# Performance work log

Measured on AMD Instinct MI355X. Metric: run time of the kernel, lower is better.

The kernel has to match this reference:

```python
import jax, jax.numpy as jnp
import numpy as np

N_NODES = 100000
N_EDGES = 1600000
IN_CH = 512
MID_CH = 64   # hard-coded mid_layer_channel in the module
OUT_CH = 40


def setup_inputs() -> dict:
    key = jax.random.key(0)
    k0, k1, k2, k3 = jax.random.split(key, 4)
    node_feature = jax.random.normal(k0, (N_NODES, IN_CH), dtype=jnp.float32)
    # edge index [2, E]: row 0 = src, row 1 = dst
    adj_list = jax.random.randint(k1, (2, N_EDGES), 0, N_NODES, dtype=jnp.int32)
    # GCNConv parameters (Glorot-ish scale)
    W1 = jax.random.normal(k2, (IN_CH, MID_CH), dtype=jnp.float32) * (1.0 / np.sqrt(IN_CH))
    b1 = jnp.zeros((MID_CH,), dtype=jnp.float32)
    W2 = jax.random.normal(k3, (MID_CH, OUT_CH), dtype=jnp.float32) * (1.0 / np.sqrt(MID_CH))
    b2 = jnp.zeros((OUT_CH,), dtype=jnp.float32)
    return {"node_feature": node_feature, "adj_list": adj_list,
            "W1": W1, "b1": b1, "W2": W2, "b2": b2}


def _gcn_conv(x, W, b, src, dst, deg_inv_sqrt, n_nodes):
    # Standard GCNConv: D^{-1/2} (A + I) D^{-1/2} (x W) + b
    h = x @ W                                             # [N, F_out]
    norm = deg_inv_sqrt[src] * deg_inv_sqrt[dst]          # [E]
    agg = jax.ops.segment_sum(h[src] * norm[:, None], dst, num_segments=n_nodes)
    agg = agg + h * (deg_inv_sqrt * deg_inv_sqrt)[:, None]  # self-loop term
    return agg + b


def reference(node_feature, adj_list, W1, b1, W2, b2):
    n = node_feature.shape[0]
    src, dst = adj_list[0], adj_list[1]
    # degree with self-loops (in-degree at dst + 1)
    deg = jax.ops.segment_sum(jnp.ones_like(dst, dtype=node_feature.dtype), dst,
                              num_segments=n) + 1.0
    deg_inv_sqrt = jax.lax.rsqrt(deg)
    h = jax.nn.elu(_gcn_conv(node_feature, W1, b1, src, dst, deg_inv_sqrt, n))
    out = _gcn_conv(h, W2, b2, src, dst, deg_inv_sqrt, n)
    return jax.nn.log_softmax(out, axis=1)
```

## Files before the change

### kernel.cpp

```cpp
#include <hip/hip_runtime.h>
#include <hip/hip_bf16.h>
#include <math.h>

#define IN_CH 512
#define MID_CH 64
#define OUT_CH 40

typedef __attribute__((ext_vector_type(8))) short short8;
typedef __attribute__((ext_vector_type(4))) float f32x4;
typedef __attribute__((ext_vector_type(2))) float f32x2;

static __device__ __forceinline__ unsigned short f2bf(float f) {
    unsigned int u = __float_as_uint(f);
    u += 0x7fffu + ((u >> 16) & 1u);
    return (unsigned short)(u >> 16);
}

__global__ void k_init(const float* __restrict__ W1, unsigned short* __restrict__ w1f,
                       int* __restrict__ cnt, int* __restrict__ esrc, int dummy_off,
                       int epad, unsigned char* __restrict__ h1q,
                       unsigned char* __restrict__ h2q, int N) {
    int i = blockIdx.x * 256 + threadIdx.x;
    if (i < epad) esrc[i] = dummy_off;
    if (i < N) cnt[i] = 0;
    if (i < IN_CH * MID_CH) {
        int k = i >> 6, c = i & 63;
        w1f[(((k >> 3) * 64) + c) * 8 + (k & 7)] = f2bf(W1[i]);
    }
    if (i < 64) {
        h1q[(size_t)N * 64 + i] = 0;
        h2q[(size_t)N * 64 + i] = 0;
    }
}

__global__ void k_countrank(const int* __restrict__ dst, int* __restrict__ cnt,
                            int* __restrict__ rank, int E) {
    int e = blockIdx.x * blockDim.x + threadIdx.x;
    if (e < E) rank[e] = atomicAdd(&cnt[dst[e]], 1);
}

__global__ void k_scanA(const int* __restrict__ cnt, int* __restrict__ rowptr,
                        int* __restrict__ bsum, float* __restrict__ dis, int N) {
    __shared__ int wsum[16];
    int i = blockIdx.x * 1024 + threadIdx.x;
    int lane = threadIdx.x & 63, wv = threadIdx.x >> 6;
    int v = (i < N) ? cnt[i] : 0;
    if (i < N) dis[i] = rsqrtf((float)v + 1.0f);
    int x = (v + 3) & ~3;
    #pragma unroll
    for (int off = 1; off < 64; off <<= 1) {
        int t = __shfl_up(x, off);
        if (lane >= off) x += t;
    }
    if (lane == 63) wsum[wv] = x;
    __syncthreads();
    if (wv == 0 && lane < 16) {
        int own = wsum[lane];
        int y = own;
        #pragma unroll
        for (int off = 1; off < 16; off <<= 1) {
            int t = __shfl_up(y, off);
            if (lane >= off) y += t;
        }
        wsum[lane] = y - own;
        if (lane == 15) bsum[blockIdx.x] = y;
    }
    __syncthreads();
    if (i < N) rowptr[i + 1] = x + wsum[wv];
}

__global__ void k_scanB(int* __restrict__ bsum, int nb) {
    __shared__ int tmp[2];
    int lane = threadIdx.x & 63, wv = threadIdx.x >> 6;
    int v = (threadIdx.x < nb) ? bsum[threadIdx.x] : 0;
    int x = v;
    #pragma unroll
    for (int off = 1; off < 64; off <<= 1) {
        int t = __shfl_up(x, off);
        if (lane >= off) x += t;
    }
    if (lane == 63) tmp[wv] = x;
    __syncthreads();
    int add = (wv == 1) ? tmp[0] : 0;
    if (threadIdx.x < nb) bsum[threadIdx.x] = x - v + add;
}

__global__ void k_scanC(int* __restrict__ rowptr, const int* __restrict__ bsum, int N) {
    int i = blockIdx.x * 1024 + threadIdx.x;
    if (i < N) rowptr[i + 1] += bsum[blockIdx.x];
    if (i == 0) rowptr[0] = 0;
}

__global__ void k_fill(const int* __restrict__ src, const int* __restrict__ dst,
                       const int* __restrict__ rank, const int* __restrict__ rowptr,
                       int* __restrict__ esrc, int E) {
    int e = blockIdx.x * blockDim.x + threadIdx.x;
    if (e < E) {
        int p = rowptr[dst[e]] + rank[e];
        esrc[p] = src[e] << 6;
    }
}

__launch_bounds__(512, 4)
__global__ void k_gemm1(const float* __restrict__ X, const unsigned short* __restrict__ w1f,
                        const float* __restrict__ dis, unsigned char* __restrict__ h1q,
                        int N) {
    __shared__ __align__(16) unsigned short wlds[IN_CH * MID_CH];
    {
        const uint4* s4 = (const uint4*)w1f;
        uint4* d4 = (uint4*)wlds;
        #pragma unroll
        for (int i = 0; i < 8; ++i)
            d4[threadIdx.x + i * 512] = s4[threadIdx.x + i * 512];
    }
    __syncthreads();

    int wave = threadIdx.x >> 6, lane = threadIdx.x & 63;
    int rbase = blockIdx.x * 128 + wave * 16;
    int g = lane >> 4;
    int arow = rbase + (lane & 15);
    if (arow > N - 1) arow = N - 1;
    const float* xp = X + (size_t)arow * IN_CH + g * 8;

    f32x4 acc[4];
    #pragma unroll
    for (int i = 0; i < 4; ++i) acc[i] = (f32x4){0.f, 0.f, 0.f, 0.f};

    float4 bx0[4], bx1[4];
    #pragma unroll
    for (int i = 0; i < 4; ++i) {
        const float4* p = (const float4*)(xp + i * 32);
        bx0[i] = p[0]; bx1[i] = p[1];
    }

    #pragma unroll
    for (int ks = 0; ks < 16; ++ks) {
        float4 x0 = bx0[ks & 3], x1 = bx1[ks & 3];
        if (ks < 12) {
            const float4* p = (const float4*)(xp + (ks + 4) * 32);
            bx0[ks & 3] = p[0]; bx1[ks & 3] = p[1];
        }
        short8 a;
        a[0] = (short)f2bf(x0.x); a[1] = (short)f2bf(x0.y);
        a[2] = (short)f2bf(x0.z); a[3] = (short)f2bf(x0.w);
        a[4] = (short)f2bf(x1.x); a[5] = (short)f2bf(x1.y);
        a[6] = (short)f2bf(x1.z); a[7] = (short)f2bf(x1.w);

        int cibase = (ks * 4 + g) * 64 + (lane & 15);
        #pragma unroll
        for (int ct = 0; ct < 4; ++ct) {
            short8 b = *((const short8*)(wlds + (size_t)(cibase + ct * 16) * 8));
            acc[ct] = __builtin_amdgcn_mfma_f32_16x16x32_bf16(a, b, acc[ct], 0, 0, 0);
        }
    }

    int colb = lane & 15;
    int rquad = rbase + (lane >> 4) * 4;
    #pragma unroll
    for (int ct = 0; ct < 4; ++ct) {
        #pragma unroll
        for (int r = 0; r < 4; ++r) {
            int row = rquad + r;
            if (row < N) {
                float v = acc[ct][r] * dis[row];
                unsigned q = __builtin_amdgcn_cvt_pk_fp8_f32(v, v, 0, false);
                h1q[(size_t)row * 64 + ct * 16 + colb] = (unsigned char)q;
            }
        }
    }
}

#define AGG_UNPACK8(Q)                                              \
    {                                                               \
        f32x2 lo_ = __builtin_amdgcn_cvt_pk_f32_fp8((Q), false);    \
        f32x2 hi_ = __builtin_amdgcn_cvt_pk_f32_fp8((Q), true);     \
        acc[0] += lo_[0]; acc[1] += lo_[1];                         \
        acc[2] += hi_[0]; acc[3] += hi_[1];                         \
    }

#define GATHER_CORE(HB)                                                 \
    f32x4 acc = (f32x4){0.f, 0.f, 0.f, 0.f};                            \
    for (int cbeg = beg; cbeg < end; cbeg += 64) {                      \
        int m = end - cbeg; if (m > 64) m = 64;      \
        int soff = esrc[cbeg + lane];                                   \
        int k4n = m >> 2;                                               \
        int k4 = 0;                                                     \
        for (; k4 + 4 <= k4n; k4 += 4) {                                \
            int o0 = __shfl(soff, (k4 + 0) * 4 + g);                    \
            int o1 = __shfl(soff, (k4 + 1) * 4 + g);                    \
            int o2 = __shfl(soff, (k4 + 2) * 4 + g);                    \
            int o3 = __shfl(soff, (k4 + 3) * 4 + g);                    \
            unsigned q0 = *(const unsigned*)((HB) + ((unsigned)o0 + cgoff)); \
            unsigned q1 = *(const unsigned*)((HB) + ((unsigned)o1 + cgoff)); \
            unsigned q2 = *(const unsigned*)((HB) + ((unsigned)o2 + cgoff)); \
            unsigned q3 = *(const unsigned*)((HB) + ((unsigned)o3 + cgoff)); \
            AGG_UNPACK8(q0) AGG_UNPACK8(q1) AGG_UNPACK8(q2) AGG_UNPACK8(q3) \
        }                                                               \
        for (; k4 < k4n; ++k4) {                                        \
            int o = __shfl(soff, k4 * 4 + g);                           \
            unsigned q = *(const unsigned*)((HB) + ((unsigned)o + cgoff)); \
            AGG_UNPACK8(q)                                              \
        }                                                               \
    }                                                                   \
    _Pragma("unroll")                                                   \
    for (int off = 32; off >= 16; off >>= 1) {                          \
        acc[0] += __shfl_xor(acc[0], off);                              \
        acc[1] += __shfl_xor(acc[1], off);                              \
        acc[2] += __shfl_xor(acc[2], off);                              \
        acc[3] += __shfl_xor(acc[3], off);                              \
    }

__launch_bounds__(256)
__global__ void k_agg1(const unsigned char* __restrict__ hq, const float* __restrict__ dis,
                       const int* __restrict__ rowptr, const int* __restrict__ esrc,
                       const float* __restrict__ b1, unsigned char* __restrict__ h2q,
                       int N) {
    int wv = threadIdx.x >> 6, lane = threadIdx.x & 63;
    int n = blockIdx.x * 4 + wv;
    if (n >= N) return;
    int g = lane >> 4, cg = lane & 15;
    int beg = rowptr[n], end = rowptr[n + 1];
    unsigned cgoff = (unsigned)(cg * 4);
    const char* hb = (const char*)hq;

    GATHER_CORE(hb)

    if (g == 0) {
        float dn = dis[n];
        unsigned qs = *(const unsigned*)(hb + ((unsigned)(n * 64) + cgoff));
        f32x2 slo = __builtin_amdgcn_cvt_pk_f32_fp8(qs, false);
        f32x2 shi = __builtin_amdgcn_cvt_pk_f32_fp8(qs, true);
        float4 b4 = *(const float4*)(b1 + cg * 4);
        float v0 = dn * (acc[0] + slo[0]) + b4.x;
        float v1 = dn * (acc[1] + slo[1]) + b4.y;
        float v2 = dn * (acc[2] + shi[0]) + b4.z;
        float v3 = dn * (acc[3] + shi[1]) + b4.w;
        v0 = v0 > 0.f ? v0 : expm1f(v0);
        v1 = v1 > 0.f ? v1 : expm1f(v1);
        v2 = v2 > 0.f ? v2 : expm1f(v2);
        v3 = v3 > 0.f ? v3 : expm1f(v3);
        unsigned w = __builtin_amdgcn_cvt_pk_fp8_f32(dn * v0, dn * v1, 0, false);
        w = __builtin_amdgcn_cvt_pk_fp8_f32(dn * v2, dn * v3, w, true);
        *(unsigned*)(h2q + (size_t)n * 64 + cg * 4) = w;
    }
}

__launch_bounds__(256)
__global__ void k_agg2(const unsigned char* __restrict__ hq, const float* __restrict__ dis,
                       const int* __restrict__ rowptr, const int* __restrict__ esrc,
                       const float* __restrict__ W2, const float* __restrict__ b2,
                       float* __restrict__ out, int N) {
    __shared__ float w2l[MID_CH * OUT_CH];
    __shared__ float vl[4 * MID_CH];
    for (int f = threadIdx.x; f < MID_CH * OUT_CH; f += 256) w2l[f] = W2[f];
    __syncthreads();

    int wv = threadIdx.x >> 6, lane = threadIdx.x & 63;
    int n = blockIdx.x * 4 + wv;
    if (n >= N) return;
    int g = lane >> 4, cg = lane & 15;
    int beg = rowptr[n], end = rowptr[n + 1];
    unsigned cgoff = (unsigned)(cg * 4);
    const char* hb = (const char*)hq;

    GATHER_CORE(hb)

    if (g == 0) {
        float dn = dis[n];
        unsigned qs = *(const unsigned*)(hb + ((unsigned)(n * 64) + cgoff));
        f32x2 slo = __builtin_amdgcn_cvt_pk_f32_fp8(qs, false);
        f32x2 shi = __builtin_amdgcn_cvt_pk_f32_fp8(qs, true);
        float4 v;
        v.x = dn * (acc[0] + slo[0]);
        v.y = dn * (acc[1] + slo[1]);
        v.z = dn * (acc[2] + shi[0]);
        v.w = dn * (acc[3] + shi[1]);
        *(float4*)&vl[wv * 64 + cg * 4] = v;
    }

    float o = (lane < OUT_CH) ? b2[lane] : 0.f;
    const float* vrow = &vl[wv * 64];
    #pragma unroll 8
    for (int c = 0; c < MID_CH; ++c)
        o += vrow[c] * w2l[c * OUT_CH + lane];

    float mx = (lane < OUT_CH) ? o : -1e30f;
    #pragma unroll
    for (int off = 32; off > 0; off >>= 1) mx = fmaxf(mx, __shfl_xor(mx, off));
    float e = (lane < OUT_CH) ? expf(o - mx) : 0.f;
    float ssum = e;
    #pragma unroll
    for (int off = 32; off > 0; off >>= 1) ssum += __shfl_xor(ssum, off);
    if (lane < OUT_CH)
        out[(size_t)n * OUT_CH + lane] = o - mx - logf(ssum);
}

extern "C" void kernel_launch(void* const* d_in, const int* in_sizes, int n_in,
                              void* d_out, int out_size, void* d_ws, size_t ws_size,
                              hipStream_t stream) {
    const float* X  = (const float*)d_in[0];
    const int* adj  = (const int*)d_in[1];
    const float* W1 = (const float*)d_in[2];
    const float* b1 = (const float*)d_in[3];
    const float* W2 = (const float*)d_in[4];
    const float* b2 = (const float*)d_in[5];
    float* out = (float*)d_out;

    int N = in_sizes[0] / IN_CH;
    int E = in_sizes[1] / 2;
    const int* srcp = adj;
    const int* dstp = adj + E;
    int nchunk = (N + 1023) / 1024;
    int epad_max = E + 3 * N + 128;

    char* ws = (char*)d_ws;
    size_t off = 0;
    int*   cnt    = (int*)(ws + off);  off += (size_t)N * sizeof(int);
    int*   rank   = (int*)(ws + off);  off += (size_t)E * sizeof(int);
    float* dis    = (float*)(ws + off); off += (size_t)N * sizeof(float);
    int*   rowptr = (int*)(ws + off);  off += ((size_t)N + 8) * sizeof(int);
    int*   bsum   = (int*)(ws + off);  off += 128 * sizeof(int);
    int*   esrc   = (int*)(ws + off);  off += (size_t)epad_max * sizeof(int);
    unsigned short* w1f = (unsigned short*)(ws + off); off += (size_t)IN_CH * MID_CH * sizeof(unsigned short);
    unsigned char* h1q = (unsigned char*)(ws + off); off += (size_t)(N + 4) * MID_CH;
    unsigned char* h2q = (unsigned char*)(ws + off); off += (size_t)(N + 4) * MID_CH;

    k_init<<<(epad_max + 255) / 256, 256, 0, stream>>>(W1, w1f, cnt, esrc, N << 6,
                                                       epad_max, h1q, h2q, N);
    k_countrank<<<(E + 255) / 256, 256, 0, stream>>>(dstp, cnt, rank, E);
    k_scanA<<<nchunk, 1024, 0, stream>>>(cnt, rowptr, bsum, dis, N);
    k_scanB<<<1, 128, 0, stream>>>(bsum, nchunk);
    k_scanC<<<nchunk, 1024, 0, stream>>>(rowptr, bsum, N);

    k_fill<<<(E + 255) / 256, 256, 0, stream>>>(srcp, dstp, rank, rowptr, esrc, E);
    k_gemm1<<<(N + 127) / 128, 512, 0, stream>>>(X, w1f, dis, h1q, N);

    int nb = (N + 3) / 4;
    k_agg1<<<nb, 256, 0, stream>>>(h1q, dis, rowptr, esrc, b1, h2q, N);
    k_agg2<<<nb, 256, 0, stream>>>(h2q, dis, rowptr, esrc, W2, b2, out, N);
}
```

Before: 282.7 us.

## Merge init with degree counting and fill with GEMM1 into shared launches

Folds the edge-count atomics into the init kernel by giving it extra persistent blocks, and moves the zeroing of the count array to a memset. The CSR fill and the first dense GEMM now share one launch with interleaved block roles, so the memory-bound scatter runs alongside the MFMA GEMM. This removes two launches and lets independent work overlap. Occupancy hint for the GEMM drops to 2 blocks, and fill blocks also reserve the 64KB of LDS.

New measurement: 297.4 us. 1.05x slower.

```diff
diff --git a/kernel.cpp b/kernel.cpp
--- a/kernel.cpp
+++ b/kernel.cpp
@@ -16,13 +16,21 @@
     return (unsigned short)(u >> 16);
 }
 
-__global__ void k_init(const float* __restrict__ W1, unsigned short* __restrict__ w1f,
-                       int* __restrict__ cnt, int* __restrict__ esrc, int dummy_off,
-                       int epad, unsigned char* __restrict__ h1q,
-                       unsigned char* __restrict__ h2q, int N) {
-    int i = blockIdx.x * 256 + threadIdx.x;
+__global__ void k_initcount(const float* __restrict__ W1, unsigned short* __restrict__ w1f,
+                            const int* __restrict__ dst, int* __restrict__ cnt,
+                            int* __restrict__ rank, int* __restrict__ esrc,
+                            int dummy_off, int epad,
+                            unsigned char* __restrict__ h1q, unsigned char* __restrict__ h2q,
+                            int N, int E, int CB) {
+    int b = blockIdx.x;
+    if (b < CB) {
+        int stride = CB * 256;
+        for (int e = b * 256 + (int)threadIdx.x; e < E; e += stride)
+            rank[e] = atomicAdd(&cnt[dst[e]], 1);
+        return;
+    }
+    int i = (b - CB) * 256 + threadIdx.x;
     if (i < epad) esrc[i] = dummy_off;
-    if (i < N) cnt[i] = 0;
     if (i < IN_CH * MID_CH) {
         int k = i >> 6, c = i & 63;
         w1f[(((k >> 3) * 64) + c) * 8 + (k & 7)] = f2bf(W1[i]);
@@ -31,12 +39,6 @@
         h1q[(size_t)N * 64 + i] = 0;
         h2q[(size_t)N * 64 + i] = 0;
     }
-}
-
-__global__ void k_countrank(const int* __restrict__ dst, int* __restrict__ cnt,
-                            int* __restrict__ rank, int E) {
-    int e = blockIdx.x * blockDim.x + threadIdx.x;
-    if (e < E) rank[e] = atomicAdd(&cnt[dst[e]], 1);
 }
 
 __global__ void k_scanA(const int* __restrict__ cnt, int* __restrict__ rowptr,
@@ -91,21 +93,30 @@
     if (i == 0) rowptr[0] = 0;
 }
 
-__global__ void k_fill(const int* __restrict__ src, const int* __restrict__ dst,
-                       const int* __restrict__ rank, const int* __restrict__ rowptr,
-                       int* __restrict__ esrc, int E) {
-    int e = blockIdx.x * blockDim.x + threadIdx.x;
-    if (e < E) {
-        int p = rowptr[dst[e]] + rank[e];
-        esrc[p] = src[e] << 6;
-    }
-}
-
-__launch_bounds__(512, 4)
-__global__ void k_gemm1(const float* __restrict__ X, const unsigned short* __restrict__ w1f,
-                        const float* __restrict__ dis, unsigned char* __restrict__ h1q,
-                        int N) {
+__launch_bounds__(512, 2)
+__global__ void k_fillgemm(const float* __restrict__ X, const unsigned short* __restrict__ w1f,
+                           const float* __restrict__ dis, unsigned char* __restrict__ h1q,
+                           int N, int FB,
+                           const int* __restrict__ src, const int* __restrict__ dst,
+                           const int* __restrict__ rank, const int* __restrict__ rowptr,
+                           int* __restrict__ esrc, int E) {
     __shared__ __align__(16) unsigned short wlds[IN_CH * MID_CH];
+    int b = blockIdx.x;
+    int gb, fb = -1;
+    if (b < 2 * FB) { if (b & 1) { fb = b >> 1; gb = -1; } else gb = b >> 1; }
+    else gb = b - FB;
+
+    if (fb >= 0) {
+        int ech = (E + FB - 1) / FB;
+        int e0 = fb * ech;
+        int e1 = e0 + ech; if (e1 > E) e1 = E;
+        for (int e = e0 + (int)threadIdx.x; e < e1; e += 512) {
+            int p = rowptr[dst[e]] + rank[e];
+            esrc[p] = src[e] << 6;
+        }
+        return;
+    }
+
     {
         const uint4* s4 = (const uint4*)w1f;
         uint4* d4 = (uint4*)wlds;
@@ -116,7 +127,7 @@
     __syncthreads();
 
     int wave = threadIdx.x >> 6, lane = threadIdx.x & 63;
-    int rbase = blockIdx.x * 128 + wave * 16;
+    int rbase = gb * 128 + wave * 16;
     int g = lane >> 4;
     int arow = rbase + (lane & 15);
     if (arow > N - 1) arow = N - 1;
@@ -149,8 +160,8 @@
         int cibase = (ks * 4 + g) * 64 + (lane & 15);
         #pragma unroll
         for (int ct = 0; ct < 4; ++ct) {
-            short8 b = *((const short8*)(wlds + (size_t)(cibase + ct * 16) * 8));
-            acc[ct] = __builtin_amdgcn_mfma_f32_16x16x32_bf16(a, b, acc[ct], 0, 0, 0);
+            short8 bb = *((const short8*)(wlds + (size_t)(cibase + ct * 16) * 8));
+            acc[ct] = __builtin_amdgcn_mfma_f32_16x16x32_bf16(a, bb, acc[ct], 0, 0, 0);
         }
     }
 
@@ -312,6 +323,9 @@
     const int* dstp = adj + E;
     int nchunk = (N + 1023) / 1024;
     int epad_max = E + 3 * N + 128;
+    int GB = (N + 127) / 128;
+    int FB = GB;
+    int CB = 512;
 
     char* ws = (char*)d_ws;
     size_t off = 0;
@@ -325,15 +339,16 @@
     unsigned char* h1q = (unsigned char*)(ws + off); off += (size_t)(N + 4) * MID_CH;
     unsigned char* h2q = (unsigned char*)(ws + off); off += (size_t)(N + 4) * MID_CH;
 
-    k_init<<<(epad_max + 255) / 256, 256, 0, stream>>>(W1, w1f, cnt, esrc, N << 6,
-                                                       epad_max, h1q, h2q, N);
-    k_countrank<<<(E + 255) / 256, 256, 0, stream>>>(dstp, cnt, rank, E);
+    hipMemsetAsync(cnt, 0, (size_t)N * sizeof(int), stream);
+    int IB = (epad_max + 255) / 256;
+    k_initcount<<<CB + IB, 256, 0, stream>>>(W1, w1f, dstp, cnt, rank, esrc, N << 6,
+                                             epad_max, h1q, h2q, N, E, CB);
     k_scanA<<<nchunk, 1024, 0, stream>>>(cnt, rowptr, bsum, dis, N);
     k_scanB<<<1, 128, 0, stream>>>(bsum, nchunk);
     k_scanC<<<nchunk, 1024, 0, stream>>>(rowptr, bsum, N);
 
-    k_fill<<<(E + 255) / 256, 256, 0, stream>>>(srcp, dstp, rank, rowptr, esrc, E);
-    k_gemm1<<<(N + 127) / 128, 512, 0, stream>>>(X, w1f, dis, h1q, N);
+    k_fillgemm<<<FB + GB, 512, 0, stream>>>(X, w1f, dis, h1q, N, FB,
+                                            srcp, dstp, rank, rowptr, esrc, E);
 
     int nb = (N + 3) / 4;
     k_agg1<<<nb, 256, 0, stream>>>(h1q, dis, rowptr, esrc, b1, h2q, N);
```
